# Optimization experiments

Measured on AMD Instinct MI355X. Metric: run time of the kernel, lower is better.

## Reference

```python
import jax, jax.numpy as jnp
import numpy as np

D_HEAD = 128


def setup_inputs() -> dict:
    key = jax.random.key(0)
    k1, k2, k3 = jax.random.split(key, 3)
    batch, num_q, seq_len, d = 16, 64, 4096, D_HEAD
    query = jax.random.normal(k1, (batch, num_q, d), dtype=jnp.float32)
    keys = jax.random.normal(k2, (batch, seq_len, d), dtype=jnp.float32)
    values = jax.random.normal(k3, (batch, seq_len, d), dtype=jnp.float32)
    return {"query": query, "keys": keys, "values": values}


def reference(query, keys, values):
    # AttentionJacobian.forward with 3D query -> compute_attention_jacobian_batched
    # J[b,q] = scale * ( sum_n a[b,q,n] v[b,n] k[b,n]^T  -  (a V)[b,q] ((a K)[b,q])^T )
    d_k = keys.shape[-1]
    scale = d_k ** (-0.5)
    scores = jnp.einsum('bqd,bnd->bqn', query, keys) * scale
    attn_weights = jax.nn.softmax(scores, axis=-1)            # (b, q, n)
    attn_outputs = jnp.einsum('bqn,bnv->bqv', attn_weights, values)
    # term1 without materializing (b, q, n, v, k): fuse as single contraction
    term1 = jnp.einsum('bqn,bnv,bnk->bqvk', attn_weights, values, keys)
    weighted_keys_sum = jnp.einsum('bqn,bnk->bqk', attn_weights, keys)
    term2 = jnp.einsum('bqv,bqk->bqvk', attn_outputs, weighted_keys_sum)
    jacobians = scale * (term1 - term2)                       # (b, q, d_v, d_k)
    return jacobians
```

## Files before the change

kernel.cpp:

```cpp
#include <hip/hip_runtime.h>
#include <stdint.h>

typedef _Float16 f16;
typedef _Float16 half4 __attribute__((ext_vector_type(4)));
typedef _Float16 half8 __attribute__((ext_vector_type(8)));
typedef float f32x4 __attribute__((ext_vector_type(4)));

#define BATCH 16
#define NQ 64
#define SL 4096
#define DH 128


__global__ __launch_bounds__(256) void kprep(const float* __restrict__ Kg,
                                             const float* __restrict__ Vg,
                                             f16* __restrict__ Kt,
                                             f16* __restrict__ Vt) {
  __shared__ f16 Ld[128][130];
  const int blk = blockIdx.x;
  const int b = blk >> 6;
  const int tensor = (blk >> 5) & 1;
  const int chunk = blk & 31;
  const float* src = tensor ? Vg : Kg;
  f16* dst = tensor ? Vt : Kt;
  const int t = threadIdx.x;
  const int n0 = chunk * 128;
  {
    const int d = t & 127;
    const int nl = t >> 7;
    const float* s = src + ((size_t)b * SL + n0 + nl) * DH + d;
    for (int it = 0; it < 64; ++it)
      Ld[d][nl + it * 2] = (f16)s[(size_t)it * 2 * DH];
  }
  __syncthreads();
  {
    const int r = t & 15;
    const int kc = (t >> 4) & 3;
    const int w = t >> 6;
    char* dstb = (char*)(dst + (size_t)b * DH * SL);
#pragma unroll
    for (int tl = 0; tl < 4; ++tl)
#pragma unroll
      for (int hh = 0; hh < 2; ++hh) {
        const int dhi = w + hh * 4;
        const int d = dhi * 16 + r;
        const int nl = tl * 32 + kc * 8;
        const half8 v = *(const half8*)&Ld[d][nl];
        *(half8*)(dstb + (size_t)(chunk * 4 + tl) * 8192 + dhi * 1024 +
                  kc * 256 + r * 16) = v;
      }
  }
}

__global__ __launch_bounds__(256) void kscore(const float* __restrict__ Q,
                                              const f16* __restrict__ Kt,
                                              f16* __restrict__ E) {
  const int blk = (blockIdx.x & 7) * 64 + (blockIdx.x >> 3);
  __shared__ float Qs[8][128];
  const int b = blk >> 5;
  const int qg = (blk >> 2) & 7;
  const int ns = blk & 3;
  const int t = threadIdx.x;
  for (int i = t; i < 8 * 128; i += 256)
    Qs[i >> 7][i & 127] = Q[((size_t)b * NQ + qg * 8 + (i >> 7)) * DH + (i & 127)];
  __syncthreads();
  const int w = t >> 6, l = t & 63;
  const int q0 = (w >> 1) * 4;
  const int nbase = ns * 1024 + (w & 1) * 512 + l * 8;
  const f16* kb = Kt + (size_t)b * DH * SL + (size_t)(nbase >> 5) * 4096 +
                  (size_t)((nbase >> 3) & 3) * 128;
  float acc[4][8] = {};
  for (int d = 0; d < DH; ++d) {
    const half8 kv = *(const half8*)(kb + (d >> 4) * 512 + (d & 15) * 8);
    float kf[8];
#pragma unroll
    for (int j = 0; j < 8; ++j) kf[j] = (float)kv[j];
#pragma unroll
    for (int qi = 0; qi < 4; ++qi) {
      const float qv = Qs[q0 + qi][d];
#pragma unroll
      for (int j = 0; j < 8; ++j) acc[qi][j] += qv * kf[j];
    }
  }
  const float scl = 0.08838834764831845f;
#pragma unroll
  for (int qi = 0; qi < 4; ++qi) {
    half8 ev;
#pragma unroll
    for (int j = 0; j < 8; ++j) ev[j] = (f16)__expf(acc[qi][j] * scl);
    *(half8*)&E[((size_t)b * NQ + qg * 8 + q0 + qi) * SL + nbase] = ev;
  }
}

__global__ __launch_bounds__(256) void kev(const f16* __restrict__ Vt,
                                           const f16* __restrict__ Kt,
                                           const f16* __restrict__ E,
                                           float* __restrict__ EVp,
                                           float* __restrict__ EKp,
                                           float* __restrict__ denomp) {
  __shared__ __align__(16) f16 Es[32][40];
  const int blk = (blockIdx.x & 7) * 32 + (blockIdx.x >> 3);
  const int b = blk >> 4;
  const int tensor = (blk >> 3) & 1;
  const int nq = (blk >> 1) & 3;
  const int qh = blk & 1;
  const char* src = (const char*)((tensor ? Kt : Vt) + (size_t)b * DH * SL);
  float* dst = (tensor ? EKp : EVp) +
               ((size_t)nq * BATCH * NQ + (size_t)b * NQ + qh * 32) * DH;
  const f16* Eb = E + ((size_t)b * NQ + qh * 32) * SL + nq * 1024;
  const int t = threadIdx.x, w = t >> 6, l = t & 63;
  const int eq = t >> 3;
  const int en = (t & 7) * 4;

  f32x4 acc[2][2] = {};
  float dsum = 0.f;

  for (int chunk = 0; chunk < 32; ++chunk) {
    const half4 ev4 = *(const half4*)(Eb + (size_t)eq * SL + chunk * 32 + en);
    *(half4*)&Es[eq][en] = ev4;
    if (!tensor)
      dsum += (float)ev4[0] + (float)ev4[1] + (float)ev4[2] + (float)ev4[3];
    __syncthreads();
    const int n0 = nq * 1024 + chunk * 32;
    const size_t gb = (size_t)(n0 >> 5) * 8192 + l * 16;
    const half8 a0 = *(const half8*)(src + gb + w * 1024);
    const half8 a1 = *(const half8*)(src + gb + (w + 4) * 1024);
    half8 b0, b1;
#pragma unroll
    for (int j = 0; j < 8; ++j) {
      b0[j] = Es[l & 15][(l >> 4) * 8 + j];
      b1[j] = Es[16 + (l & 15)][(l >> 4) * 8 + j];
    }
    acc[0][0] = __builtin_amdgcn_mfma_f32_16x16x32_f16(a0, b0, acc[0][0], 0, 0, 0);
    acc[0][1] = __builtin_amdgcn_mfma_f32_16x16x32_f16(a0, b1, acc[0][1], 0, 0, 0);
    acc[1][0] = __builtin_amdgcn_mfma_f32_16x16x32_f16(a1, b0, acc[1][0], 0, 0, 0);
    acc[1][1] = __builtin_amdgcn_mfma_f32_16x16x32_f16(a1, b1, acc[1][1], 0, 0, 0);
    __syncthreads();
  }

#pragma unroll
  for (int sv2 = 0; sv2 < 2; ++sv2)
#pragma unroll
    for (int qsub = 0; qsub < 2; ++qsub) {
      const int q = qsub * 16 + (l & 15);
      const int row = (w + sv2 * 4) * 16 + (l >> 4) * 4;
      *(f32x4*)&dst[(size_t)q * DH + row] = acc[sv2][qsub];
    }

  if (!tensor) {
    dsum += __shfl_xor(dsum, 1);
    dsum += __shfl_xor(dsum, 2);
    dsum += __shfl_xor(dsum, 4);
    if ((t & 7) == 0)
      denomp[(size_t)nq * BATCH * NQ + (size_t)b * NQ + qh * 32 + eq] = dsum;
  }
}

__global__ __launch_bounds__(512, 2) void kjac(
    const f16* __restrict__ Vt, const f16* __restrict__ Kt,
    const f16* __restrict__ E, const float* __restrict__ EV,
    const float* __restrict__ EK, const float* __restrict__ denomp,
    float* __restrict__ out) {
  const int blk = (blockIdx.x & 7) * 32 + (blockIdx.x >> 3);
  const int b = blk >> 4;
  const int q0 = (blk & 15) * 4;
  const int t = threadIdx.x, w = t >> 6, l = t & 63;
  const int sA = (w >> 2) * 4;
  const int sB = (w & 3) * 2;
  const char* vtb = (const char*)(Vt + (size_t)b * DH * SL) + sA * 1024 + l * 16;
  const char* ktb = (const char*)(Kt + (size_t)b * DH * SL) + sB * 1024 + l * 16;
  const f16* Eb = E + ((size_t)b * NQ + q0) * SL + (l >> 4) * 8;

  f32x4 acc[4][4][2] = {};
  half8 vfA[4], kfA[2], efA[4], vfB[4], kfB[2], efB[4];

#define LOADF(vf, kf, ef, tile)                                              \
  {                                                                          \
    const size_t gb = (size_t)(tile) * 8192;                                 \
    _Pragma("unroll") for (int i = 0; i < 4; ++i) vf[i] =                    \
        *(const half8*)(vtb + gb + i * 1024);                                \
    _Pragma("unroll") for (int j = 0; j < 2; ++j) kf[j] =                    \
        *(const half8*)(ktb + gb + j * 1024);                                \
    _Pragma("unroll") for (int q = 0; q < 4; ++q) ef[q] =                    \
        *(const half8*)(Eb + (size_t)q * SL + (tile) * 32);                  \
  }

#define MFMA32(vf, kf, ef)                                                   \
  {                                                                          \
    __builtin_amdgcn_s_setprio(1);                                           \
    _Pragma("unroll") for (int q = 0; q < 4; ++q) {                          \
      const half8 uk0 = ef[q] * kf[0];                                       \
      const half8 uk1 = ef[q] * kf[1];                                       \
      _Pragma("unroll") for (int i = 0; i < 4; ++i) {                        \
        acc[q][i][0] = __builtin_amdgcn_mfma_f32_16x16x32_f16(               \
            vf[i], uk0, acc[q][i][0], 0, 0, 0);                              \
        acc[q][i][1] = __builtin_amdgcn_mfma_f32_16x16x32_f16(               \
            vf[i], uk1, acc[q][i][1], 0, 0, 0);                              \
      }                                                                      \
    }                                                                        \
    __builtin_amdgcn_s_setprio(0);                                           \
  }

  LOADF(vfA, kfA, efA, 0)
  for (int tt = 0; tt < 126; tt += 2) {
    LOADF(vfB, kfB, efB, tt + 1)
    MFMA32(vfA, kfA, efA)
    LOADF(vfA, kfA, efA, tt + 2)
    MFMA32(vfB, kfB, efB)
  }
  LOADF(vfB, kfB, efB, 127)
  MFMA32(vfA, kfA, efA)
  MFMA32(vfB, kfB, efB)
#undef LOADF
#undef MFMA32

  const float scl = 0.08838834764831845f;
  const size_t PS = (size_t)BATCH * NQ * DH;
  const size_t DS = (size_t)BATCH * NQ;
#pragma unroll
  for (int q = 0; q < 4; ++q) {
    const size_t qi = (size_t)b * NQ + q0 + q;
    float den = 0.f;
#pragma unroll
    for (int p = 0; p < 4; ++p) den += denomp[p * DS + qi];
    const float invd = 1.0f / den;
    const float* evq = EV + qi * DH;
    const float* ekq = EK + qi * DH;
    float* ob = out + qi * DH * DH;
#pragma unroll
    for (int i = 0; i < 4; ++i) {
      const int row0 = (sA + i) * 16 + (l >> 4) * 4;
      f32x4 ev4 = *(const f32x4*)&evq[row0];
#pragma unroll
      for (int p = 1; p < 4; ++p) ev4 += *(const f32x4*)&evq[p * PS + row0];
#pragma unroll
      for (int j = 0; j < 2; ++j) {
        const int col = (sB + j) * 16 + (l & 15);
        float ek = ekq[col];
#pragma unroll
        for (int p = 1; p < 4; ++p) ek += ekq[p * PS + col];
#pragma unroll
        for (int r = 0; r < 4; ++r)
          ob[(size_t)(row0 + r) * DH + col] =
              scl * invd * (acc[q][i][j][r] - invd * ev4[r] * ek);
      }
    }
  }
}

extern "C" void kernel_launch(void* const* d_in, const int* in_sizes, int n_in,
                              void* d_out, int out_size, void* d_ws,
                              size_t ws_size, hipStream_t stream) {
  const float* Q = (const float*)d_in[0];
  const float* K = (const float*)d_in[1];
  const float* V = (const float*)d_in[2];
  float* out = (float*)d_out;

  f16* Vt = (f16*)d_ws;
  f16* Kt = Vt + (size_t)BATCH * DH * SL;
  f16* Ef = Kt + (size_t)BATCH * DH * SL;
  float* EVp = (float*)(Ef + (size_t)BATCH * NQ * SL);
  float* EKp = EVp + 4 * (size_t)BATCH * NQ * DH;
  float* denomp = EKp + 4 * (size_t)BATCH * NQ * DH;

  kprep<<<1024, 256, 0, stream>>>(K, V, Kt, Vt);
  kscore<<<512, 256, 0, stream>>>(Q, Kt, Ef);
  kev<<<256, 256, 0, stream>>>(Vt, Kt, Ef, EVp, EKp, denomp);
  kjac<<<256, 512, 0, stream>>>(Vt, Kt, Ef, EVp, EKp, denomp, out);
}
```

Before: 178.9 us.

## Fuse EV/EK reductions into Jacobian kernel and denominator into score kernel

Removes the separate kev kernel: the softmax denominator is now summed in kscore as the exponentials are written, and the weighted V and K sums are accumulated inside kjac's main loop with fdot2 dot products on the fragments already loaded for the MFMAs. Cross-lane shuffles then redistribute those sums to the epilogue layout. This avoids an extra pass over E, V and K plus a launch and partial-sum buffers, at the cost of added VALU work interleaved with the MFMA loop and more registers.

```diff
diff --git a/kernel.cpp b/kernel.cpp
--- a/kernel.cpp
+++ b/kernel.cpp
@@ -2,6 +2,7 @@
 #include <stdint.h>
 
 typedef _Float16 f16;
+typedef _Float16 half2_t __attribute__((ext_vector_type(2)));
 typedef _Float16 half4 __attribute__((ext_vector_type(4)));
 typedef _Float16 half8 __attribute__((ext_vector_type(8)));
 typedef float f32x4 __attribute__((ext_vector_type(4)));
@@ -11,6 +12,30 @@
 #define SL 4096
 #define DH 128
 
+
+#if __has_builtin(__builtin_amdgcn_fdot2)
+#define DOT8(accv, a, b)                                                     \
+  {                                                                          \
+    accv = __builtin_amdgcn_fdot2(__builtin_shufflevector(a, a, 0, 1),       \
+                                  __builtin_shufflevector(b, b, 0, 1), accv, \
+                                  false);                                    \
+    accv = __builtin_amdgcn_fdot2(__builtin_shufflevector(a, a, 2, 3),       \
+                                  __builtin_shufflevector(b, b, 2, 3), accv, \
+                                  false);                                    \
+    accv = __builtin_amdgcn_fdot2(__builtin_shufflevector(a, a, 4, 5),       \
+                                  __builtin_shufflevector(b, b, 4, 5), accv, \
+                                  false);                                    \
+    accv = __builtin_amdgcn_fdot2(__builtin_shufflevector(a, a, 6, 7),       \
+                                  __builtin_shufflevector(b, b, 6, 7), accv, \
+                                  false);                                    \
+  }
+#else
+#define DOT8(accv, a, b)                                                     \
+  {                                                                          \
+    _Pragma("unroll") for (int _k = 0; _k < 8; ++_k) accv +=                 \
+        (float)a[_k] * (float)b[_k];                                         \
+  }
+#endif
 
 __global__ __launch_bounds__(256) void kprep(const float* __restrict__ Kg,
                                              const float* __restrict__ Vg,
@@ -54,9 +79,11 @@
 
 __global__ __launch_bounds__(256) void kscore(const float* __restrict__ Q,
                                               const f16* __restrict__ Kt,
-                                              f16* __restrict__ E) {
+                                              f16* __restrict__ E,
+                                              float* __restrict__ denomp) {
   const int blk = (blockIdx.x & 7) * 64 + (blockIdx.x >> 3);
   __shared__ float Qs[8][128];
+  __shared__ float wsum[4][4];
   const int b = blk >> 5;
   const int qg = (blk >> 2) & 7;
   const int ns = blk & 3;
@@ -86,80 +113,27 @@
 #pragma unroll
   for (int qi = 0; qi < 4; ++qi) {
     half8 ev;
-#pragma unroll
-    for (int j = 0; j < 8; ++j) ev[j] = (f16)__expf(acc[qi][j] * scl);
+    float ds = 0.f;
+#pragma unroll
+    for (int j = 0; j < 8; ++j) {
+      ev[j] = (f16)__expf(acc[qi][j] * scl);
+      ds += (float)ev[j];
+    }
     *(half8*)&E[((size_t)b * NQ + qg * 8 + q0 + qi) * SL + nbase] = ev;
-  }
-}
-
-__global__ __launch_bounds__(256) void kev(const f16* __restrict__ Vt,
-                                           const f16* __restrict__ Kt,
-                                           const f16* __restrict__ E,
-                                           float* __restrict__ EVp,
-                                           float* __restrict__ EKp,
-                                           float* __restrict__ denomp) {
-  __shared__ __align__(16) f16 Es[32][40];
-  const int blk = (blockIdx.x & 7) * 32 + (blockIdx.x >> 3);
-  const int b = blk >> 4;
-  const int tensor = (blk >> 3) & 1;
-  const int nq = (blk >> 1) & 3;
-  const int qh = blk & 1;
-  const char* src = (const char*)((tensor ? Kt : Vt) + (size_t)b * DH * SL);
-  float* dst = (tensor ? EKp : EVp) +
-               ((size_t)nq * BATCH * NQ + (size_t)b * NQ + qh * 32) * DH;
-  const f16* Eb = E + ((size_t)b * NQ + qh * 32) * SL + nq * 1024;
-  const int t = threadIdx.x, w = t >> 6, l = t & 63;
-  const int eq = t >> 3;
-  const int en = (t & 7) * 4;
-
-  f32x4 acc[2][2] = {};
-  float dsum = 0.f;
-
-  for (int chunk = 0; chunk < 32; ++chunk) {
-    const half4 ev4 = *(const half4*)(Eb + (size_t)eq * SL + chunk * 32 + en);
-    *(half4*)&Es[eq][en] = ev4;
-    if (!tensor)
-      dsum += (float)ev4[0] + (float)ev4[1] + (float)ev4[2] + (float)ev4[3];
-    __syncthreads();
-    const int n0 = nq * 1024 + chunk * 32;
-    const size_t gb = (size_t)(n0 >> 5) * 8192 + l * 16;
-    const half8 a0 = *(const half8*)(src + gb + w * 1024);
-    const half8 a1 = *(const half8*)(src + gb + (w + 4) * 1024);
-    half8 b0, b1;
-#pragma unroll
-    for (int j = 0; j < 8; ++j) {
-      b0[j] = Es[l & 15][(l >> 4) * 8 + j];
-      b1[j] = Es[16 + (l & 15)][(l >> 4) * 8 + j];
-    }
-    acc[0][0] = __builtin_amdgcn_mfma_f32_16x16x32_f16(a0, b0, acc[0][0], 0, 0, 0);
-    acc[0][1] = __builtin_amdgcn_mfma_f32_16x16x32_f16(a0, b1, acc[0][1], 0, 0, 0);
-    acc[1][0] = __builtin_amdgcn_mfma_f32_16x16x32_f16(a1, b0, acc[1][0], 0, 0, 0);
-    acc[1][1] = __builtin_amdgcn_mfma_f32_16x16x32_f16(a1, b1, acc[1][1], 0, 0, 0);
-    __syncthreads();
-  }
-
-#pragma unroll
-  for (int sv2 = 0; sv2 < 2; ++sv2)
-#pragma unroll
-    for (int qsub = 0; qsub < 2; ++qsub) {
-      const int q = qsub * 16 + (l & 15);
-      const int row = (w + sv2 * 4) * 16 + (l >> 4) * 4;
-      *(f32x4*)&dst[(size_t)q * DH + row] = acc[sv2][qsub];
-    }
-
-  if (!tensor) {
-    dsum += __shfl_xor(dsum, 1);
-    dsum += __shfl_xor(dsum, 2);
-    dsum += __shfl_xor(dsum, 4);
-    if ((t & 7) == 0)
-      denomp[(size_t)nq * BATCH * NQ + (size_t)b * NQ + qh * 32 + eq] = dsum;
+    for (int off = 1; off < 64; off <<= 1) ds += __shfl_xor(ds, off);
+    if (l == 0) wsum[w][qi] = ds;
+  }
+  __syncthreads();
+  if (t < 8) {
+    const int hw = (t >> 2) * 2;
+    denomp[(size_t)ns * BATCH * NQ + (size_t)b * NQ + qg * 8 + t] =
+        wsum[hw][t & 3] + wsum[hw + 1][t & 3];
   }
 }
 
 __global__ __launch_bounds__(512, 2) void kjac(
     const f16* __restrict__ Vt, const f16* __restrict__ Kt,
-    const f16* __restrict__ E, const float* __restrict__ EV,
-    const float* __restrict__ EK, const float* __restrict__ denomp,
+    const f16* __restrict__ E, const float* __restrict__ denomp,
     float* __restrict__ out) {
   const int blk = (blockIdx.x & 7) * 32 + (blockIdx.x >> 3);
   const int b = blk >> 4;
@@ -172,6 +146,8 @@
   const f16* Eb = E + ((size_t)b * NQ + q0) * SL + (l >> 4) * 8;
 
   f32x4 acc[4][4][2] = {};
+  float evr[4][4] = {};
+  float ekr[4][2] = {};
   half8 vfA[4], kfA[2], efA[4], vfB[4], kfB[2], efB[4];
 
 #define LOADF(vf, kf, ef, tile)                                              \
@@ -191,11 +167,14 @@
     _Pragma("unroll") for (int q = 0; q < 4; ++q) {                          \
       const half8 uk0 = ef[q] * kf[0];                                       \
       const half8 uk1 = ef[q] * kf[1];                                       \
+      DOT8(ekr[q][0], ef[q], kf[0])                                          \
+      DOT8(ekr[q][1], ef[q], kf[1])                                          \
       _Pragma("unroll") for (int i = 0; i < 4; ++i) {                        \
         acc[q][i][0] = __builtin_amdgcn_mfma_f32_16x16x32_f16(               \
             vf[i], uk0, acc[q][i][0], 0, 0, 0);                              \
         acc[q][i][1] = __builtin_amdgcn_mfma_f32_16x16x32_f16(               \
             vf[i], uk1, acc[q][i][1], 0, 0, 0);                              \
+        DOT8(evr[q][i], ef[q], vf[i])                                        \
       }                                                                      \
     }                                                                        \
     __builtin_amdgcn_s_setprio(0);                                           \
@@ -214,8 +193,21 @@
 #undef LOADF
 #undef MFMA32
 
+#pragma unroll
+  for (int q = 0; q < 4; ++q) {
+#pragma unroll
+    for (int i = 0; i < 4; ++i) {
+      evr[q][i] += __shfl_xor(evr[q][i], 16);
+      evr[q][i] += __shfl_xor(evr[q][i], 32);
+    }
+#pragma unroll
+    for (int j = 0; j < 2; ++j) {
+      ekr[q][j] += __shfl_xor(ekr[q][j], 16);
+      ekr[q][j] += __shfl_xor(ekr[q][j], 32);
+    }
+  }
+
   const float scl = 0.08838834764831845f;
-  const size_t PS = (size_t)BATCH * NQ * DH;
   const size_t DS = (size_t)BATCH * NQ;
 #pragma unroll
   for (int q = 0; q < 4; ++q) {
@@ -224,25 +216,22 @@
 #pragma unroll
     for (int p = 0; p < 4; ++p) den += denomp[p * DS + qi];
     const float invd = 1.0f / den;
-    const float* evq = EV + qi * DH;
-    const float* ekq = EK + qi * DH;
     float* ob = out + qi * DH * DH;
+    const int rbase = (l >> 4) * 4;
 #pragma unroll
     for (int i = 0; i < 4; ++i) {
-      const int row0 = (sA + i) * 16 + (l >> 4) * 4;
-      f32x4 ev4 = *(const f32x4*)&evq[row0];
-#pragma unroll
-      for (int p = 1; p < 4; ++p) ev4 += *(const f32x4*)&evq[p * PS + row0];
+      const int row0 = (sA + i) * 16 + rbase;
+      float evv[4];
+#pragma unroll
+      for (int r = 0; r < 4; ++r) evv[r] = __shfl(evr[q][i], rbase + r);
 #pragma unroll
       for (int j = 0; j < 2; ++j) {
         const int col = (sB + j) * 16 + (l & 15);
-        float ek = ekq[col];
-#pragma unroll
-        for (int p = 1; p < 4; ++p) ek += ekq[p * PS + col];
+        const float ek = ekr[q][j];
 #pragma unroll
         for (int r = 0; r < 4; ++r)
           ob[(size_t)(row0 + r) * DH + col] =
-              scl * invd * (acc[q][i][j][r] - invd * ev4[r] * ek);
+              scl * invd * (acc[q][i][j][r] - invd * evv[r] * ek);
       }
     }
   }
@@ -259,12 +248,9 @@
   f16* Vt = (f16*)d_ws;
   f16* Kt = Vt + (size_t)BATCH * DH * SL;
   f16* Ef = Kt + (size_t)BATCH * DH * SL;
-  float* EVp = (float*)(Ef + (size_t)BATCH * NQ * SL);
-  float* EKp = EVp + 4 * (size_t)BATCH * NQ * DH;
-  float* denomp = EKp + 4 * (size_t)BATCH * NQ * DH;
+  float* denomp = (float*)(Ef + (size_t)BATCH * NQ * SL);
 
   kprep<<<1024, 256, 0, stream>>>(K, V, Kt, Vt);
-  kscore<<<512, 256, 0, stream>>>(Q, Kt, Ef);
-  kev<<<256, 256, 0, stream>>>(Vt, Kt, Ef, EVp, EKp, denomp);
-  kjac<<<256, 512, 0, stream>>>(Vt, Kt, Ef, EVp, EKp, denomp, out);
-}
+  kscore<<<512, 256, 0, stream>>>(Q, Kt, Ef, denomp);
+  kjac<<<256, 512, 0, stream>>>(Vt, Kt, Ef, denomp, out);
+}
```

Result: slower. 229.9 us (+28.5%).
